# Performance work log

Measured on AMD Instinct MI355X. Metric: run time of the kernel, lower is better.

The kernel has to match this reference:

```python
import jax, jax.numpy as jnp
import numpy as np

B, N, HID = 1, 2048, 2048
NH, NKV, HD = 16, 4, 128
GROUPS = NH // NKV
CHUNK = 64          # get_valid_chunk_size(B*NH*N=32768, 64) == 64
MAG = 0.5
GATE_NORM = 16.0


def setup_inputs() -> dict:
    key = jax.random.key(0)
    ks = jax.random.split(key, 5)
    s = 0.02
    return {
        "hidden_states": jax.random.normal(ks[0], (B, N, HID), jnp.float32),
        "Wq": jax.random.normal(ks[1], (NH * HD, HID), jnp.float32) * s,
        "Wk": jax.random.normal(ks[2], (NKV * HD, HID), jnp.float32) * s,
        "Wv": jax.random.normal(ks[3], (NKV * HD, HID), jnp.float32) * s,
        "Wo": jax.random.normal(ks[4], (HID, NH * HD), jnp.float32) * s,
    }


def _delta_rule_chunked(q, k, v, beta, chunk_size):
    """Chunkwise delta-rule linear attention (DeltaNet chunk form).
    q,k,v,beta: [T, d] flattened tokens; returns (o [T,d], final_state [d,d])."""
    T, d = q.shape
    n = T // chunk_size
    qc, kc, vc, bc = (x.reshape(n, chunk_size, d) for x in (q, k, v, beta))
    kb = kc * bc                       # beta-weighted keys
    vb = vc * bc                       # beta-weighted values
    strict = jnp.tril(jnp.ones((chunk_size, chunk_size), bool), -1)
    eye = jnp.eye(chunk_size, dtype=q.dtype)
    # A = I + strictly-lower(k_beta k^T); unit lower triangular -> invert by triangular solve
    A = eye + jnp.where(strict, jnp.einsum('ncd,nkd->nck', kb, kc), 0.0)
    Tinv = jax.vmap(lambda a: jax.scipy.linalg.solve_triangular(a, eye, lower=True))(A)
    w = Tinv @ kb                      # [n, C, d]
    u = Tinv @ vb                      # [n, C, d]
    causal = jnp.tril(jnp.ones((chunk_size, chunk_size), bool))

    def step(S, inp):
        qi, ki, wi, ui = inp           # each [C, d]
        u_i = ui - wi @ S              # correct pseudo-values by inter-chunk state
        attn = jnp.where(causal, qi @ ki.T, 0.0)
        o = qi @ S + attn @ u_i
        return S + ki.T @ u_i, o

    S0 = jnp.zeros((d, d), q.dtype)
    Sf, o = jax.lax.scan(step, S0, (qc, kc, w, u))
    return o.reshape(T, d), Sf


def _forward(hidden_states, Wq, Wk, Wv, Wo):
    q = hidden_states @ Wq.T           # [B, N, NH*HD]
    k = hidden_states @ Wk.T           # [B, N, NKV*HD]
    v = hidden_states @ Wv.T           # [B, N, NKV*HD]
    g = k                              # AdaptiveAvgPool1d(512 -> 512) is identity
    qh = q.reshape(B, N, NH, HD).transpose(0, 2, 1, 3)   # b h n d
    kh = k.reshape(B, N, NKV, HD).transpose(0, 2, 1, 3)
    vh = v.reshape(B, N, NKV, HD).transpose(0, 2, 1, 3)
    gh = g.reshape(B, N, NKV, HD).transpose(0, 2, 1, 3)
    rep = lambda x: jnp.repeat(x, GROUPS, axis=1)        # repeat_kv
    khr, vhr, ghr = rep(kh), rep(vh), rep(gh)

    # linear-attention path: softmax feature maps + logsigmoid gate
    ql = jax.nn.softmax(qh, axis=-1).astype(jnp.float32)
    kl = jax.nn.softmax(khr, axis=-1).astype(jnp.float32)
    gl = (jax.nn.log_sigmoid(ghr) / GATE_NORM).astype(jnp.float32)
    vl = vhr.astype(jnp.float32)
    flat = lambda x: x.reshape(B * NH * N, HD)
    o_lin, _ = _delta_rule_chunked(flat(ql), flat(kl), flat(vl), flat(gl), CHUNK)
    o_lin = o_lin.reshape(B, NH, N, HD).transpose(0, 2, 1, 3).reshape(B, N, NH * HD)
    o_lin = o_lin @ Wo.T

    # base (vanilla causal softmax) attention path
    scores = jnp.einsum('bhnd,bhmd->bhnm', qh, khr) * (HD ** -0.5)
    cmask = jnp.tril(jnp.ones((N, N), bool))
    scores = jnp.where(cmask[None, None], scores, jnp.finfo(scores.dtype).min)
    attn = jax.nn.softmax(scores, axis=-1)
    o_base = jnp.einsum('bhnm,bhmd->bhnd', attn, vhr)
    o_base = o_base.transpose(0, 2, 1, 3).reshape(B, N, NH * HD) @ Wo.T

    return MAG * o_lin + (1.0 - MAG) * o_base


def reference(hidden_states, Wq, Wk, Wv, Wo):
    return _forward(hidden_states, Wq, Wk, Wv, Wo)
```

## Files before the change

kernel.cpp:

```cpp
#include <hip/hip_runtime.h>
#include <hip/hip_bf16.h>

typedef unsigned short u16;
typedef unsigned int u32;
typedef __bf16 bf16x8 __attribute__((ext_vector_type(8)));
typedef float f32x4 __attribute__((ext_vector_type(4)));

#define MFMA16(a,b,c) __builtin_amdgcn_mfma_f32_16x16x32_bf16((a),(b),(c),0,0,0)

__device__ __forceinline__ u16 f2bf(float f){
  u32 u = __builtin_bit_cast(u32, f);
  u32 r = (u + 0x7fffu + ((u >> 16) & 1u)) >> 16;
  return (u16)r;
}
__device__ __forceinline__ float bf2f(u16 h){
  u32 u = ((u32)h) << 16;
  return __builtin_bit_cast(float, u);
}
__device__ __forceinline__ void splitbf(float x, u16& hi, u16& lo){
  hi = f2bf(x);
  lo = f2bf(x - bf2f(hi));
}
__device__ __forceinline__ void gload_lds16(const u16* g, u16* l){
  __builtin_amdgcn_global_load_lds((__attribute__((address_space(1))) void*)(g),
                                   (__attribute__((address_space(3))) void*)(l), 16, 0, 0);
}
__device__ __forceinline__ const u16* selu(const u16* barr, const u16* parr, int i){
  return (i < 128) ? (barr + (size_t)i*16384) : (parr + (size_t)(i-128)*16384);
}
__device__ __forceinline__ const float* self32(const float* barr, const float* parr, int i){
  return (i < 128) ? (barr + (size_t)i*16384) : (parr + (size_t)(i-128)*16384);
}
__device__ __forceinline__ float* slotp(float* p1, float* p2, int s){
  return (s < 381) ? (p1 + (size_t)s*16512) : (p2 + (size_t)(s-381)*16512);
}
__device__ __forceinline__ const float* slotpc(const float* p1, const float* p2, int s){
  return (s < 381) ? (p1 + (size_t)s*16512) : (p2 + (size_t)(s-381)*16512);
}

constexpr size_t OF_HSBF   = 0;
constexpr size_t OF_WQKVBF = 8388608;
constexpr size_t OF_WOBF   = 20971520;
constexpr size_t OF_QKV    = 29360128;
constexpr size_t OF_QBF    = 54525952;
constexpr size_t OF_KBF    = 62914560;
constexpr size_t OF_VT     = 65011712;
constexpr size_t OF_QLB    = 67108864;
constexpr size_t OF_KLF    = 75497472;
constexpr size_t OF_KLB    = 79691776;
constexpr size_t OF_GLF    = 81788928;
constexpr size_t OF_TINV   = 85983232;
constexpr size_t OF_WF     = 88080384;
constexpr size_t OF_WB     = 92274688;
constexpr size_t OF_U0     = 94371840;
constexpr size_t OF_SJ     = 111149056;
constexpr size_t OF_OMIX   = 127926272;
constexpr size_t OF_OMIXB  = 144703488;
constexpr size_t OF_ADF  = 102760448;
constexpr size_t OF_ABTF = OF_OMIX;
constexpr size_t OF_ADH  = OF_OMIX + 8388608;
constexpr size_t OF_ADL  = OF_OMIX + 12582912;
constexpr size_t OF_ADTH = OF_OMIXB;
constexpr size_t OF_ADTL = OF_OMIXB + 4194304;
constexpr size_t OF_ABTH = OF_KLF;
constexpr size_t OF_ABTL = OF_GLF;
constexpr size_t OF_BDF  = OF_QKV;
constexpr size_t OF_BBTF = OF_QKV + 8388608;
constexpr size_t OF_BDH  = OF_QKV + 16777216;
constexpr size_t OF_BDL  = OF_QKV + 20971520;
constexpr size_t OF_BDTH = OF_HSBF;
constexpr size_t OF_BDTL = OF_HSBF + 4194304;
constexpr size_t OF_BBTH = OF_WQKVBF;
constexpr size_t OF_BBTL = OF_WQKVBF + 4194304;
constexpr size_t OF_TTF  = OF_TINV;
constexpr size_t OF_TTH  = OF_WQKVBF + 8388608;
constexpr size_t OF_TTL  = OF_WQKVBF + 8912896;
constexpr size_t OF_PDF  = OF_ADF;
constexpr size_t OF_PBTF = OF_ADF + 1048576;
constexpr size_t OF_PDH  = OF_ADF + 2097152;
constexpr size_t OF_PDL  = OF_ADF + 2621440;
constexpr size_t OF_PDTH = OF_ADF + 3145728;
constexpr size_t OF_PDTL = OF_ADF + 3670016;
constexpr size_t OF_PBTH = OF_ADF + 4194304;
constexpr size_t OF_PBTL = OF_ADF + 4718592;
constexpr size_t OF_APART1 = OF_QKV;
constexpr size_t OF_APART2 = OF_OMIXB;
constexpr size_t OF_OBF = 0;

struct CompJobs { int a[8]; int b[8]; int d[8]; };

__global__ void k_f2ball(const float* __restrict__ hs, const float* __restrict__ Wq,
                         const float* __restrict__ Wk, const float* __restrict__ Wv,
                         const float* __restrict__ Wo, u16* __restrict__ hs_bf,
                         u16* __restrict__ wqkv_bf, u16* __restrict__ wo_bf){
  int bid = blockIdx.x;
  const float* src; u16* dst; int off;
  if(bid < 4096){ src = hs; dst = hs_bf; off = bid; }
  else if(bid < 8192){ src = Wq; dst = wqkv_bf; off = bid - 4096; }
  else if(bid < 9216){ src = Wk; dst = wqkv_bf + 2048*2048; off = bid - 8192; }
  else if(bid < 10240){ src = Wv; dst = wqkv_bf + 2560*2048; off = bid - 9216; }
  else { src = Wo; dst = wo_bf; off = bid - 10240; }
  int i = (off*256 + threadIdx.x) * 4;
  f32x4 v = *(const f32x4*)(src + i);
  u32 w0 = (u32)f2bf(v[0]) | ((u32)f2bf(v[1]) << 16);
  u32 w1 = (u32)f2bf(v[2]) | ((u32)f2bf(v[3]) << 16);
  *(u32*)(dst + i) = w0;
  *(u32*)(dst + i + 2) = w1;
}

__global__ __launch_bounds__(256) void k_gemm(const u16* __restrict__ A, const u16* __restrict__ B,
                                              float* __restrict__ C, int K, int N){
  __shared__ u16 aL[128*32];
  __shared__ u16 bL[128*32];
  int lin = blockIdx.y * gridDim.x + blockIdx.x;
  int nwg = gridDim.x * gridDim.y;
  int s = (lin & 7) * (nwg >> 3) + (lin >> 3);
  int bn = s % gridDim.x, bm = s / gridDim.x;
  int tid = threadIdx.x, lane = tid & 63, w = tid >> 6;
  int wm = w >> 1, wn = w & 1;
  f32x4 acc[4][4] = {};
  int nK = K >> 5;
  const u16* Abase = A + (size_t)bm * 128 * K;
  const u16* Bbase = B + (size_t)bn * 128 * K;
  for(int kt = 0; kt < nK; ++kt){
    __syncthreads();
    #pragma unroll
    for(int t = 0; t < 2; ++t){
      int row = t*64 + w*16 + (lane >> 2);
      int kc = (lane & 3) * 8;
      gload_lds16(Abase + (size_t)row*K + kt*32 + kc, &aL[(t*64 + w*16)*32]);
      gload_lds16(Bbase + (size_t)row*K + kt*32 + kc, &bL[(t*64 + w*16)*32]);
    }
    __syncthreads();
    bf16x8 af[4], bf[4];
    #pragma unroll
    for(int i = 0; i < 4; ++i){
      af[i] = *(const bf16x8*)&aL[(wm*64 + i*16 + (lane & 15))*32 + ((lane >> 4) << 3)];
      bf[i] = *(const bf16x8*)&bL[(wn*64 + i*16 + (lane & 15))*32 + ((lane >> 4) << 3)];
    }
    #pragma unroll
    for(int i = 0; i < 4; ++i)
      #pragma unroll
      for(int j = 0; j < 4; ++j)
        acc[i][j] = MFMA16(af[i], bf[j], acc[i][j]);
  }
  #pragma unroll
  for(int i = 0; i < 4; ++i)
    #pragma unroll
    for(int j = 0; j < 4; ++j)
      #pragma unroll
      for(int r = 0; r < 4; ++r){
        int row = bm*128 + wm*64 + i*16 + ((lane >> 4) << 2) + r;
        int col = bn*128 + wn*64 + j*16 + (lane & 15);
        C[(size_t)row * N + col] = acc[i][j][r];
      }
}

__global__ __launch_bounds__(256) void k_linvt(const float* __restrict__ qkv, u16* qbf, u16* qlb,
                                               u16* kbf, float* klf, u16* klb, float* glf,
                                               u16* __restrict__ vT){
  __shared__ float t[64][65];
  int bid = blockIdx.x;
  if(bid < 10240){
    int gtask = bid * 4 + (threadIdx.x >> 6);
    int lane = threadIdx.x & 63;
    int n = gtask / 20, tt = gtask % 20;
    const float* row = (tt < 16) ? (qkv + (size_t)n*3072 + tt*128)
                                 : (qkv + (size_t)n*3072 + 2048 + (tt-16)*128);
    float v0 = row[lane], v1 = row[lane + 64];
    float m = fmaxf(v0, v1);
    #pragma unroll
    for(int o = 1; o < 64; o <<= 1) m = fmaxf(m, __shfl_xor(m, o, 64));
    float e0 = __expf(v0 - m), e1 = __expf(v1 - m);
    float s = e0 + e1;
    #pragma unroll
    for(int o = 1; o < 64; o <<= 1) s += __shfl_xor(s, o, 64);
    float r0 = e0 / s, r1 = e1 / s;
    if(tt < 16){
      size_t base = ((size_t)tt*2048 + n) * 128;
      qbf[base + lane] = f2bf(v0); qbf[base + 64 + lane] = f2bf(v1);
      qlb[base + lane] = f2bf(r0); qlb[base + 64 + lane] = f2bf(r1);
    } else {
      int g = tt - 16;
      size_t base = ((size_t)g*2048 + n) * 128;
      kbf[base + lane] = f2bf(v0); kbf[base + 64 + lane] = f2bf(v1);
      klf[base + lane] = r0;       klf[base + 64 + lane] = r1;
      klb[base + lane] = f2bf(r0); klb[base + 64 + lane] = f2bf(r1);
      float g0 = (fminf(v0, 0.f) - log1pf(__expf(-fabsf(v0)))) * (1.f/16.f);
      float g1 = (fminf(v1, 0.f) - log1pf(__expf(-fabsf(v1)))) * (1.f/16.f);
      glf[base + lane] = g0; glf[base + 64 + lane] = g1;
    }
  } else {
    int v = bid - 10240;
    int nt = v & 31, dt = (v >> 5) & 1, g = v >> 6;
    int tid = threadIdx.x;
    {
      int r = tid >> 2, c0 = (tid & 3) * 16;
      const float* src = qkv + (size_t)(nt*64 + r)*3072 + 2560 + g*128 + dt*64 + c0;
      #pragma unroll
      for(int q = 0; q < 16; q += 4){
        f32x4 vv = *(const f32x4*)(src + q);
        t[r][c0+q] = vv[0]; t[r][c0+q+1] = vv[1]; t[r][c0+q+2] = vv[2]; t[r][c0+q+3] = vv[3];
      }
    }
    __syncthreads();
    {
      int d = tid >> 2, c0 = (tid & 3) * 16;
      u16* dst = vT + ((size_t)g*128 + dt*64 + d)*2048 + (size_t)nt*64 + c0;
      #pragma unroll
      for(int half = 0; half < 2; ++half){
        int b = c0 + half*8;
        u32 w0 = (u32)f2bf(t[b+0][d]) | ((u32)f2bf(t[b+1][d]) << 16);
        u32 w1 = (u32)f2bf(t[b+2][d]) | ((u32)f2bf(t[b+3][d]) << 16);
        u32 w2 = (u32)f2bf(t[b+4][d]) | ((u32)f2bf(t[b+5][d]) << 16);
        u32 w3 = (u32)f2bf(t[b+6][d]) | ((u32)f2bf(t[b+7][d]) << 16);
        *(uint4*)(dst + half*8) = make_uint4(w0, w1, w2, w3);
      }
    }
  }
}

__global__ __launch_bounds__(256) void k_prep1(const float* __restrict__ klf, const float* __restrict__ glf,
                                               float* __restrict__ tinv){
  __shared__ float KlT[128][68];
  __shared__ float Kb[64][132];
  __shared__ float Am[64][68];
  __shared__ float XT[64][68];
  int idx = blockIdx.x, g = idx >> 5, c = idx & 31, tid = threadIdx.x;
  size_t base = ((size_t)g*2048 + c*64) * 128;
  {
    int r = tid >> 2, d0 = (tid & 3) * 32;
    #pragma unroll
    for(int dd = 0; dd < 32; dd += 4){
      f32x4 kv = *(const f32x4*)(klf + base + r*128 + d0 + dd);
      f32x4 gv = *(const f32x4*)(glf + base + r*128 + d0 + dd);
      KlT[d0+dd][r] = kv[0]; KlT[d0+dd+1][r] = kv[1]; KlT[d0+dd+2][r] = kv[2]; KlT[d0+dd+3][r] = kv[3];
      f32x4 kb = kv * gv;
      *(f32x4*)&Kb[r][d0+dd] = kb;
    }
  }
  __syncthreads();
  {
    int i = tid >> 2, j0 = (tid & 3) * 16;
    f32x4 s[4] = {};
    for(int d = 0; d < 128; ++d){
      float kb = Kb[i][d];
      #pragma unroll
      for(int q = 0; q < 4; ++q){
        f32x4 kl = *(const f32x4*)&KlT[d][j0 + q*4];
        s[q] += kb * kl;
      }
    }
    #pragma unroll
    for(int q = 0; q < 4; ++q) *(f32x4*)&Am[i][j0 + q*4] = s[q];
  }
  __syncthreads();
  if(tid < 64){
    int cc = tid;
    float x0 = (cc == 0) ? 1.f : 0.f;
    XT[cc][0] = x0;
    tinv[(size_t)idx*4096 + cc] = x0;
    for(int i = 1; i < 64; ++i){
      float s = (i == cc) ? 1.f : 0.f;
      int i4 = i & ~3;
      for(int jj = 0; jj < i4; jj += 4){
        f32x4 av = *(const f32x4*)&Am[i][jj];
        f32x4 xv = *(const f32x4*)&XT[cc][jj];
        s -= av[0]*xv[0] + av[1]*xv[1] + av[2]*xv[2] + av[3]*xv[3];
      }
      for(int jj = i4; jj < i; ++jj) s -= Am[i][jj] * XT[cc][jj];
      XT[cc][i] = s;
      tinv[(size_t)idx*4096 + i*64 + cc] = s;
    }
  }
}

__global__ __launch_bounds__(256) void k_prep2a(const float* __restrict__ klf, const float* __restrict__ glf,
                                                const float* __restrict__ qkv, const float* __restrict__ tinv,
                                                float* __restrict__ wf, u16* __restrict__ wb, float* __restrict__ u0f){
  __shared__ float Ti[64][68];
  __shared__ float B1[64][132];
  __shared__ float B2[64][132];
  int idx = blockIdx.x, g = idx >> 5, c = idx & 31, tid = threadIdx.x;
  size_t base = ((size_t)g*2048 + c*64) * 128;
  {
    int r = tid >> 2, d0 = (tid & 3) * 32;
    #pragma unroll
    for(int dd = 0; dd < 32; dd += 4){
      f32x4 kv = *(const f32x4*)(klf + base + r*128 + d0 + dd);
      f32x4 gv = *(const f32x4*)(glf + base + r*128 + d0 + dd);
      f32x4 vv = *(const f32x4*)(qkv + (size_t)(c*64 + r)*3072 + 2560 + g*128 + d0 + dd);
      *(f32x4*)&B1[r][d0+dd] = kv * gv;
      *(f32x4*)&B2[r][d0+dd] = vv * gv;
    }
    int c0 = (tid & 3) * 16;
    #pragma unroll
    for(int q = 0; q < 16; q += 4)
      *(f32x4*)&Ti[r][c0+q] = *(const f32x4*)(tinv + (size_t)idx*4096 + r*64 + c0 + q);
  }
  __syncthreads();
  int i = tid >> 2, cc0 = (tid & 3) * 32;
  f32x4 wa[8] = {}; f32x4 ua[8] = {};
  for(int jj = 0; jj < 64; ++jj){
    float a = Ti[i][jj];
    #pragma unroll
    for(int q = 0; q < 8; ++q){
      f32x4 b1 = *(const f32x4*)&B1[jj][cc0 + q*4];
      f32x4 b2 = *(const f32x4*)&B2[jj][cc0 + q*4];
      wa[q] += a * b1; ua[q] += a * b2;
    }
  }
  #pragma unroll
  for(int q = 0; q < 8; ++q){
    *(f32x4*)(wf + (size_t)idx*8192 + i*128 + cc0 + q*4) = wa[q];
    *(f32x4*)(u0f + (size_t)idx*8192 + i*128 + cc0 + q*4) = ua[q];
    u32 w0 = (u32)f2bf(wa[q][0]) | ((u32)f2bf(wa[q][1]) << 16);
    u32 w1 = (u32)f2bf(wa[q][2]) | ((u32)f2bf(wa[q][3]) << 16);
    u32* dst = (u32*)(wb + (size_t)idx*8192 + i*128 + cc0 + q*4);
    dst[0] = w0; dst[1] = w1;
  }
}

__global__ __launch_bounds__(256) void k_prep2b(const float* __restrict__ klf, const float* __restrict__ wf,
                                                const float* __restrict__ u0f,
                                                float* __restrict__ dF, u16* __restrict__ dH, u16* __restrict__ dL,
                                                u16* __restrict__ dTH, u16* __restrict__ dTL,
                                                float* __restrict__ btF, u16* __restrict__ btH, u16* __restrict__ btL){
  __shared__ float Kl[64][132];
  __shared__ float Wm[64][132];
  __shared__ float Um[64][132];
  int idx = blockIdx.x, g = idx >> 5, c = idx & 31, tid = threadIdx.x;
  size_t base = ((size_t)g*2048 + c*64) * 128;
  {
    int r = tid >> 2, d0 = (tid & 3) * 32;
    #pragma unroll
    for(int dd = 0; dd < 32; dd += 4){
      *(f32x4*)&Kl[r][d0+dd] = *(const f32x4*)(klf + base + r*128 + d0 + dd);
      *(f32x4*)&Wm[r][d0+dd] = *(const f32x4*)(wf + (size_t)idx*8192 + r*128 + d0 + dd);
      *(f32x4*)&Um[r][d0+dd] = *(const f32x4*)(u0f + (size_t)idx*8192 + r*128 + d0 + dd);
    }
  }
  __syncthreads();
  int a = tid >> 1, b0 = (tid & 1) * 64;
  f32x4 pa[16] = {}; f32x4 ca[16] = {};
  for(int r = 0; r < 64; ++r){
    float ka = Kl[r][a];
    float ua = Um[r][a];
    #pragma unroll
    for(int q = 0; q < 16; ++q){
      f32x4 wv = *(const f32x4*)&Wm[r][b0 + q*4];
      f32x4 kv = *(const f32x4*)&Kl[r][b0 + q*4];
      pa[q] += ka * wv;
      ca[q] += ua * kv;
    }
  }
  size_t ob = (size_t)idx * 16384;
  #pragma unroll
  for(int q = 0; q < 16; ++q){
    #pragma unroll
    for(int e = 0; e < 4; ++e){
      int b = b0 + q*4 + e;
      float dv = -pa[q][e];
      u16 dh, dl; splitbf(dv, dh, dl);
      dF[ob + a*128 + b] = dv;
      dH[ob + a*128 + b] = dh;
      dL[ob + a*128 + b] = dl;
      dTH[ob + (size_t)b*128 + a] = dh;
      dTL[ob + (size_t)b*128 + a] = dl;
      float cv = ca[q][e];
      u16 ch, cl; splitbf(cv, ch, cl);
      btF[ob + a*128 + b] = cv;
      btH[ob + a*128 + b] = ch;
      btL[ob + a*128 + b] = cl;
    }
  }
}

__global__ __launch_bounds__(256) void k_ks(
    const float* __restrict__ sDF, const u16* __restrict__ sDH, const u16* __restrict__ sDL,
    const u16* __restrict__ sDTH, const u16* __restrict__ sDTL,
    const float* __restrict__ sBF, const u16* __restrict__ sBH, const u16* __restrict__ sBL,
    float* __restrict__ dDF, u16* __restrict__ dDH, u16* __restrict__ dDL,
    u16* __restrict__ dDTH, u16* __restrict__ dDTL,
    float* __restrict__ dBF, u16* __restrict__ dBH, u16* __restrict__ dBL, int off){
  __shared__ float T[128][132];
  int c = blockIdx.x, g = blockIdx.y, z = blockIdx.z;
  int idx = g*32 + c, tid = threadIdx.x;
  size_t base = (size_t)idx * 16384;
  if(c < off){
    if(z == 0){
      for(int i = tid; i < 4096; i += 256) ((uint4*)(dDF + base))[i] = ((const uint4*)(sDF + base))[i];
      for(int i = tid; i < 2048; i += 256){
        ((uint4*)(dDH + base))[i] = ((const uint4*)(sDH + base))[i];
        ((uint4*)(dDL + base))[i] = ((const uint4*)(sDL + base))[i];
        ((uint4*)(dDTH + base))[i] = ((const uint4*)(sDTH + base))[i];
        ((uint4*)(dDTL + base))[i] = ((const uint4*)(sDTL + base))[i];
      }
    } else {
      for(int i = tid; i < 4096; i += 256) ((uint4*)(dBF + base))[i] = ((const uint4*)(sBF + base))[i];
      for(int i = tid; i < 2048; i += 256){
        ((uint4*)(dBH + base))[i] = ((const uint4*)(sBH + base))[i];
        ((uint4*)(dBL + base))[i] = ((const uint4*)(sBL + base))[i];
      }
    }
    return;
  }
  size_t blo = (size_t)(idx - off) * 16384;
  int lane = tid & 63, w = tid >> 6;
  const u16 *Ah, *Al, *Bh, *Bl;
  if(z == 0){ Ah = sDH + base; Al = sDL + base; Bh = sDTH + blo; Bl = sDTL + blo; }
  else      { Ah = sBH + blo;  Al = sBL + blo;  Bh = sDH + base; Bl = sDL + base; }
  f32x4 acc[2][8] = {};
  #pragma unroll
  for(int ks = 0; ks < 4; ++ks){
    bf16x8 ah[2], al[2], bh[8], bl[8];
    #pragma unroll
    for(int mt = 0; mt < 2; ++mt){
      int ro = (w*32 + mt*16 + (lane & 15))*128 + ks*32 + ((lane >> 4) << 3);
      ah[mt] = *(const bf16x8*)(Ah + ro);
      al[mt] = *(const bf16x8*)(Al + ro);
    }
    #pragma unroll
    for(int nt = 0; nt < 8; ++nt){
      int ro = (nt*16 + (lane & 15))*128 + ks*32 + ((lane >> 4) << 3);
      bh[nt] = *(const bf16x8*)(Bh + ro);
      bl[nt] = *(const bf16x8*)(Bl + ro);
    }
    #pragma unroll
    for(int mt = 0; mt < 2; ++mt)
      #pragma unroll
      for(int nt = 0; nt < 8; ++nt)
        acc[mt][nt] = MFMA16(ah[mt], bh[nt],
                      MFMA16(ah[mt], bl[nt],
                      MFMA16(al[mt], bh[nt], acc[mt][nt])));
  }
  if(z == 0){
    #pragma unroll
    for(int mt = 0; mt < 2; ++mt)
      #pragma unroll
      for(int nt = 0; nt < 8; ++nt)
        #pragma unroll
        for(int r = 0; r < 4; ++r){
          int row = w*32 + mt*16 + ((lane >> 4) << 2) + r;
          int col = nt*16 + (lane & 15);
          float v = acc[mt][nt][r] + sDF[base + row*128 + col] + sDF[blo + row*128 + col];
          dDF[base + row*128 + col] = v;
          u16 hi, lo; splitbf(v, hi, lo);
          dDH[base + row*128 + col] = hi;
          dDL[base + row*128 + col] = lo;
          T[row][col] = v;
        }
    __syncthreads();
    int tcol = tid >> 1, half = tid & 1;
    for(int m = 0; m < 64; ++m){
      float v = T[half*64 + m][tcol];
      u16 hi, lo; splitbf(v, hi, lo);
      dDTH[base + (size_t)tcol*128 + half*64 + m] = hi;
      dDTL[base + (size_t)tcol*128 + half*64 + m] = lo;
    }
  } else {
    #pragma unroll
    for(int mt = 0; mt < 2; ++mt)
      #pragma unroll
      for(int nt = 0; nt < 8; ++nt)
        #pragma unroll
        for(int r = 0; r < 4; ++r){
          int row = w*32 + mt*16 + ((lane >> 4) << 2) + r;
          int col = nt*16 + (lane & 15);
          float v = acc[mt][nt][r] + sBF[base + row*128 + col] + sBF[blo + row*128 + col];
          dBF[base + row*128 + col] = v;
          u16 hi, lo; splitbf(v, hi, lo);
          dBH[base + row*128 + col] = hi;
          dBL[base + row*128 + col] = lo;
        }
  }
}

__device__ __forceinline__ void comp_mfma(const u16* Ah, const u16* Al, const u16* Bh, const u16* Bl,
                                          f32x4 (&acc)[2][8], int lane, int w){
  #pragma unroll
  for(int ks = 0; ks < 4; ++ks){
    bf16x8 ah[2], al[2], bh[8], bl[8];
    #pragma unroll
    for(int mt = 0; mt < 2; ++mt){
      int ro = (w*32 + mt*16 + (lane & 15))*128 + ks*32 + ((lane >> 4) << 3);
      ah[mt] = *(const bf16x8*)(Ah + ro);
      al[mt] = *(const bf16x8*)(Al + ro);
    }
    #pragma unroll
    for(int nt = 0; nt < 8; ++nt){
      int ro = (nt*16 + (lane & 15))*128 + ks*32 + ((lane >> 4) << 3);
      bh[nt] = *(const bf16x8*)(Bh + ro);
      bl[nt] = *(const bf16x8*)(Bl + ro);
    }
    #pragma unroll
    for(int mt = 0; mt < 2; ++mt)
      #pragma unroll
      for(int nt = 0; nt < 8; ++nt)
        acc[mt][nt] = MFMA16(ah[mt], bh[nt],
                      MFMA16(ah[mt], bl[nt],
                      MFMA16(al[mt], bh[nt], acc[mt][nt])));
  }
}

__global__ __launch_bounds__(256) void k_comp(
    const float* __restrict__ bDF, const u16* __restrict__ bDH, const u16* __restrict__ bDL,
    const u16* __restrict__ bDTH, const u16* __restrict__ bDTL,
    const float* __restrict__ bBTF, const u16* __restrict__ bBTH, const u16* __restrict__ bBTL,
    float* __restrict__ pDF, u16* __restrict__ pDH, u16* __restrict__ pDL,
    u16* __restrict__ pDTH, u16* __restrict__ pDTL,
    float* __restrict__ pBTF, u16* __restrict__ pBTH, u16* __restrict__ pBTL,
    CompJobs jobs){
  __shared__ float T[128][132];
  int job = blockIdx.x, z = blockIdx.y, tid = threadIdx.x;
  int a = jobs.a[job], b = jobs.b[job], d = jobs.d[job] - 128;
  size_t ob = (size_t)d * 16384;
  int lane = tid & 63, w = tid >> 6;
  const u16 *Ah, *Al, *Bh, *Bl;
  const float *F1, *F2;
  if(z == 0){
    Ah = selu(bDH, pDH, a);  Al = selu(bDL, pDL, a);
    Bh = selu(bDTH, pDTH, b); Bl = selu(bDTL, pDTL, b);
    F1 = self32(bDF, pDF, a); F2 = self32(bDF, pDF, b);
  } else {
    Ah = selu(bBTH, pBTH, b); Al = selu(bBTL, pBTL, b);
    Bh = selu(bDH, pDH, a);   Bl = selu(bDL, pDL, a);
    F1 = self32(bBTF, pBTF, a); F2 = self32(bBTF, pBTF, b);
  }
  for(int i = tid*4; i < 16384; i += 1024){
    f32x4 v1 = *(const f32x4*)(F1 + i);
    f32x4 v2 = *(const f32x4*)(F2 + i);
    f32x4 sv = v1 + v2;
    int row = i >> 7, col = i & 127;
    *(f32x4*)&T[row][col] = sv;
  }
  __syncthreads();
  f32x4 acc[2][8] = {};
  comp_mfma(Ah, Al, Bh, Bl, acc, lane, w);
  if(z == 0){
    #pragma unroll
    for(int mt = 0; mt < 2; ++mt)
      #pragma unroll
      for(int nt = 0; nt < 8; ++nt)
        #pragma unroll
        for(int r = 0; r < 4; ++r){
          int row = w*32 + mt*16 + ((lane >> 4) << 2) + r;
          int col = nt*16 + (lane & 15);
          float v = acc[mt][nt][r] + T[row][col];
          pDF[ob + row*128 + col] = v;
          u16 hi, lo; splitbf(v, hi, lo);
          pDH[ob + row*128 + col] = hi;
          pDL[ob + row*128 + col] = lo;
          T[row][col] = v;
        }
    __syncthreads();
    int tcol = tid >> 1, half = tid & 1;
    for(int m = 0; m < 64; ++m){
      float v = T[half*64 + m][tcol];
      u16 hi, lo; splitbf(v, hi, lo);
      pDTH[ob + (size_t)tcol*128 + half*64 + m] = hi;
      pDTL[ob + (size_t)tcol*128 + half*64 + m] = lo;
    }
  } else {
    #pragma unroll
    for(int mt = 0; mt < 2; ++mt)
      #pragma unroll
      for(int nt = 0; nt < 8; ++nt)
        #pragma unroll
        for(int r = 0; r < 4; ++r){
          int row = w*32 + mt*16 + ((lane >> 4) << 2) + r;
          int col = nt*16 + (lane & 15);
          float v = acc[mt][nt][r] + T[row][col];
          pBTF[ob + row*128 + col] = v;
          u16 hi, lo; splitbf(v, hi, lo);
          pBTH[ob + row*128 + col] = hi;
          pBTL[ob + row*128 + col] = lo;
        }
  }
}

__global__ __launch_bounds__(256) void k_heads(
    const u16* __restrict__ bDH, const u16* __restrict__ bDL,
    const float* __restrict__ bBTF, const u16* __restrict__ bBTH, const u16* __restrict__ bBTL,
    const u16* __restrict__ pDH, const u16* __restrict__ pDL,
    const float* __restrict__ pBTF, const u16* __restrict__ pBTH, const u16* __restrict__ pBTL,
    float* __restrict__ ttF, u16* __restrict__ ttH, u16* __restrict__ ttL, u16* __restrict__ sj){
  __shared__ float T[128][132];
  int h = blockIdx.x, g = h >> 2, i0 = h & 3;
  int tid = threadIdx.x, lane = tid & 63, w = tid >> 6;
  int psi = (g == 0) ? -1 : (g == 1 ? 136 : (g == 2 ? 140 : 142));
  int phi = (i0 == 0) ? -1 : (i0 == 1 ? g*32 + 31 : (i0 == 2 ? 128 + g : 132 + g));
  const float* Pf = (psi >= 0) ? self32(bBTF, pBTF, psi) : nullptr;
  const float* Ff = (phi >= 0) ? self32(bBTF, pBTF, phi) : nullptr;
  for(int i = tid*4; i < 16384; i += 1024){
    f32x4 sv = {};
    if(Pf) sv += *(const f32x4*)(Pf + i);
    if(Ff) sv += *(const f32x4*)(Ff + i);
    int row = i >> 7, col = i & 127;
    *(f32x4*)&T[row][col] = sv;
  }
  __syncthreads();
  f32x4 acc[2][8] = {};
  if(psi >= 0 && phi >= 0)
    comp_mfma(selu(bBTH,pBTH,psi), selu(bBTL,pBTL,psi), selu(bDH,pDH,phi), selu(bDL,pDL,phi), acc, lane, w);
  #pragma unroll
  for(int mt = 0; mt < 2; ++mt)
    #pragma unroll
    for(int nt = 0; nt < 8; ++nt)
      #pragma unroll
      for(int r = 0; r < 4; ++r){
        int row = w*32 + mt*16 + ((lane >> 4) << 2) + r;
        int col = nt*16 + (lane & 15);
        float v = acc[mt][nt][r] + T[row][col];
        u16 hi, lo; splitbf(v, hi, lo);
        size_t o = (size_t)h*16384 + row*128 + col;
        ttF[o] = v; ttH[o] = hi; ttL[o] = lo;
        sj[(size_t)(h*32)*16384 + row*128 + col] = hi;
      }
}

__global__ __launch_bounds__(256) void k_expand(const u16* __restrict__ bDH, const u16* __restrict__ bDL,
                                                const float* __restrict__ bBF, const float* __restrict__ ttF,
                                                const u16* __restrict__ ttH, const u16* __restrict__ ttL,
                                                u16* __restrict__ sj){
  int j = blockIdx.x;
  int c = j & 31;
  if(c == 0) return;
  int h = j >> 5, g = h >> 2;
  size_t obase = (size_t)j * 16384;
  size_t mb = (size_t)(g*32 + c - 1) * 16384;
  size_t tb = (size_t)h * 16384;
  int tid = threadIdx.x, lane = tid & 63, w = tid >> 6;
  f32x4 acc[2][8] = {};
  comp_mfma(ttH + tb, ttL + tb, bDH + mb, bDL + mb, acc, lane, w);
  #pragma unroll
  for(int mt = 0; mt < 2; ++mt)
    #pragma unroll
    for(int nt = 0; nt < 8; ++nt)
      #pragma unroll
      for(int r = 0; r < 4; ++r){
        int row = w*32 + mt*16 + ((lane >> 4) << 2) + r;
        int col = nt*16 + (lane & 15);
        float v = acc[mt][nt][r] + ttF[tb + row*128 + col] + bBF[mb + row*128 + col];
        sj[obase + row*128 + col] = f2bf(v);
      }
}

__global__ __launch_bounds__(256) void k_olin(const u16* __restrict__ qlb, const u16* __restrict__ klb,
                                              const u16* __restrict__ wb, const float* __restrict__ u0f,
                                              const u16* __restrict__ sj, float* __restrict__ omix){
  __shared__ u16 ut[128*64];
  __shared__ u16 pl[4][16*64];
  int j = blockIdx.x;
  int h = j >> 5, c = j & 31, g = h >> 2, idx = g*32 + c;
  int tid = threadIdx.x, lane = tid & 63, w = tid >> 6;
  const u16* Sj = sj + (size_t)j * 16384;
  const u16* Q  = qlb + ((size_t)h*2048 + c*64) * 128;
  const u16* Kc = klb + ((size_t)g*2048 + c*64) * 128;
  const u16* W  = wb + (size_t)idx * 8192;
  const float* U0 = u0f + (size_t)idx * 8192;
  bf16x8 aq[4], aw[4];
  #pragma unroll
  for(int ks = 0; ks < 4; ++ks){
    aq[ks] = *(const bf16x8*)(Q + (w*16 + (lane & 15))*128 + ks*32 + ((lane >> 4) << 3));
    aw[ks] = *(const bf16x8*)(W + (w*16 + (lane & 15))*128 + ks*32 + ((lane >> 4) << 3));
  }
  f32x4 t1[8] = {}, ui[8] = {};
  #pragma unroll
  for(int ks = 0; ks < 4; ++ks)
    #pragma unroll
    for(int nt = 0; nt < 8; ++nt){
      bf16x8 b = *(const bf16x8*)(Sj + (nt*16 + (lane & 15))*128 + ks*32 + ((lane >> 4) << 3));
      t1[nt] = MFMA16(aq[ks], b, t1[nt]);
      ui[nt] = MFMA16(aw[ks], b, ui[nt]);
    }
  f32x4 sc[4] = {};
  #pragma unroll
  for(int ks = 0; ks < 4; ++ks)
    #pragma unroll
    for(int nt = 0; nt < 4; ++nt){
      bf16x8 b = *(const bf16x8*)(Kc + (nt*16 + (lane & 15))*128 + ks*32 + ((lane >> 4) << 3));
      sc[nt] = MFMA16(aq[ks], b, sc[nt]);
    }
  #pragma unroll
  for(int nt = 0; nt < 4; ++nt)
    #pragma unroll
    for(int r = 0; r < 4; ++r){
      int row = ((lane >> 4) << 2) + r;
      int col = nt*16 + (lane & 15);
      int grow = w*16 + row;
      float v = (col <= grow) ? sc[nt][r] : 0.f;
      int bo = (row*128 + col*2) ^ ((row & 7) << 4);
      *(u16*)((char*)&pl[w][0] + bo) = f2bf(v);
    }
  #pragma unroll
  for(int nt = 0; nt < 8; ++nt)
    #pragma unroll
    for(int r = 0; r < 4; ++r){
      int kv = w*16 + ((lane >> 4) << 2) + r;
      int d  = nt*16 + (lane & 15);
      float v = U0[kv*128 + d] - ui[nt][r];
      int bo = (d*128 + kv*2) ^ ((d & 7) << 4);
      *(u16*)((char*)ut + bo) = f2bf(v);
    }
  __syncthreads();
  f32x4 o2[8] = {};
  #pragma unroll
  for(int ks2 = 0; ks2 < 2; ++ks2){
    int row = lane & 15;
    int boA = (row*128 + ks2*64 + ((lane >> 4) << 4)) ^ ((row & 7) << 4);
    bf16x8 a = *(const bf16x8*)((const char*)&pl[w][0] + boA);
    #pragma unroll
    for(int nt = 0; nt < 8; ++nt){
      int d = nt*16 + (lane & 15);
      int boB = (d*128 + ks2*64 + ((lane >> 4) << 4)) ^ ((d & 7) << 4);
      bf16x8 b = *(const bf16x8*)((const char*)ut + boB);
      o2[nt] = MFMA16(a, b, o2[nt]);
    }
  }
  #pragma unroll
  for(int nt = 0; nt < 8; ++nt)
    #pragma unroll
    for(int r = 0; r < 4; ++r){
      int grow = c*64 + w*16 + ((lane >> 4) << 2) + r;
      int d = nt*16 + (lane & 15);
      omix[(size_t)grow*2048 + h*128 + d] = 0.5f * (t1[nt][r] + o2[nt][r]);
    }
}

__global__ __launch_bounds__(256) void k_attn(const u16* __restrict__ qbf, const u16* __restrict__ kbf,
                                              const u16* __restrict__ vT, const float* __restrict__ omix,
                                              u16* __restrict__ obf,
                                              float* __restrict__ part1, float* __restrict__ part2){
  __shared__ u16 pl[4][2560];
  int rb = blockIdx.x;
  int bid = (rb & 7) * 80 + (rb >> 3);
  int h = bid / 40, j = bid % 40;
  int qB, kt0, kt1, slot = -1;
  if(j < 4){ qB = j; kt0 = 0; kt1 = 4*(qB+1); }
  else {
    int jj = j - 4; int seg;
    if(jj < 8){ qB = 4 + (jj >> 1); seg = jj & 1; }
    else if(jj < 20){ int q = jj - 8; qB = 8 + q/3; seg = q - (qB-8)*3; }
    else { int q = jj - 20; qB = 12 + (q >> 2); seg = q & 3; }
    slot = h*36 + jj;
    kt0 = seg*16;
    int full = 4*(qB+1);
    kt1 = (kt0 + 16 < full) ? kt0 + 16 : full;
  }
  int g = h >> 2;
  int tid = threadIdx.x, lane = tid & 63, w = tid >> 6;
  const u16* K = kbf + (size_t)g*2048*128;
  const u16* V = vT + (size_t)g*128*2048;
  bf16x8 aq[2][4];
  #pragma unroll
  for(int m = 0; m < 2; ++m){
    const u16* Q = qbf + ((size_t)h*2048 + qB*128 + w*32 + m*16) * 128;
    #pragma unroll
    for(int ks = 0; ks < 4; ++ks)
      aq[m][ks] = *(const bf16x8*)(Q + (lane & 15)*128 + ks*32 + ((lane >> 4) << 3));
  }
  f32x4 acc[2][8] = {};
  float lsum[2][4] = {};
  const float scale = 0.08838834764831845f;
  int qr0[2];
  #pragma unroll
  for(int m = 0; m < 2; ++m) qr0[m] = qB*128 + w*32 + m*16 + ((lane >> 4) << 2);
  u16* plw = &pl[w][0];
  bf16x8 kb[8];
  #pragma unroll
  for(int ct = 0; ct < 2; ++ct)
    #pragma unroll
    for(int ks = 0; ks < 4; ++ks)
      kb[ct*4+ks] = *(const bf16x8*)(K + (size_t)(kt0*32 + ct*16 + (lane & 15))*128 + ks*32 + ((lane >> 4) << 3));
  int buf = 0;
  for(int kt = kt0; kt < kt1; ++kt){
    f32x4 s[2][2] = {};
    #pragma unroll
    for(int m = 0; m < 2; ++m)
      #pragma unroll
      for(int ct = 0; ct < 2; ++ct)
        #pragma unroll
        for(int ks = 0; ks < 4; ++ks)
          s[m][ct] = MFMA16(aq[m][ks], kb[ct*4+ks], s[m][ct]);
    bf16x8 kbn[8];
    if(kt + 1 < kt1){
      #pragma unroll
      for(int ct = 0; ct < 2; ++ct)
        #pragma unroll
        for(int ks = 0; ks < 4; ++ks)
          kbn[ct*4+ks] = *(const bf16x8*)(K + (size_t)((kt+1)*32 + ct*16 + (lane & 15))*128 + ks*32 + ((lane >> 4) << 3));
    }
    bf16x8 bv[8];
    #pragma unroll
    for(int nt = 0; nt < 8; ++nt)
      bv[nt] = *(const bf16x8*)(V + (size_t)(nt*16 + (lane & 15))*2048 + kt*32 + ((lane >> 4) << 3));
    #pragma unroll
    for(int m = 0; m < 2; ++m)
      #pragma unroll
      for(int ct = 0; ct < 2; ++ct)
        #pragma unroll
        for(int r = 0; r < 4; ++r){
          int col = kt*32 + ct*16 + (lane & 15);
          float p = (col <= qr0[m] + r) ? __expf(s[m][ct][r] * scale) : 0.f;
          lsum[m][r] += p;
          int row = m*16 + ((lane >> 4) << 2) + r;
          *(u16*)((char*)plw + buf*2560 + row*80 + (ct*16 + (lane & 15))*2) = f2bf(p);
        }
    __builtin_amdgcn_s_setprio(1);
    #pragma unroll
    for(int m = 0; m < 2; ++m){
      bf16x8 ap = *(const bf16x8*)((const char*)plw + buf*2560 + (m*16 + (lane & 15))*80 + ((lane >> 4) << 4));
      #pragma unroll
      for(int nt = 0; nt < 8; ++nt)
        acc[m][nt] = MFMA16(ap, bv[nt], acc[m][nt]);
    }
    __builtin_amdgcn_s_setprio(0);
    #pragma unroll
    for(int i = 0; i < 8; ++i) kb[i] = kbn[i];
    buf ^= 1;
  }
  #pragma unroll
  for(int m = 0; m < 2; ++m)
    #pragma unroll
    for(int r = 0; r < 4; ++r){
      float v = lsum[m][r];
      v += __shfl_xor(v, 1, 64); v += __shfl_xor(v, 2, 64);
      v += __shfl_xor(v, 4, 64); v += __shfl_xor(v, 8, 64);
      lsum[m][r] = v;
    }
  if(slot < 0){
    #pragma unroll
    for(int m = 0; m < 2; ++m)
      #pragma unroll
      for(int nt = 0; nt < 8; ++nt)
        #pragma unroll
        for(int r = 0; r < 4; ++r){
          int row = qB*128 + w*32 + m*16 + ((lane >> 4) << 2) + r;
          int d = nt*16 + (lane & 15);
          size_t o = (size_t)row*2048 + h*128 + d;
          float fin = omix[o] + 0.5f * acc[m][nt][r] / lsum[m][r];
          obf[o] = f2bf(fin);
        }
  } else {
    float* P = slotp(part1, part2, slot);
    #pragma unroll
    for(int m = 0; m < 2; ++m)
      #pragma unroll
      for(int nt = 0; nt < 8; ++nt)
        #pragma unroll
        for(int r = 0; r < 4; ++r){
          int row = w*32 + m*16 + ((lane >> 4) << 2) + r;
          int d = nt*16 + (lane & 15);
          P[(size_t)row*128 + d] = acc[m][nt][r];
        }
    if((lane & 15) == 0)
      #pragma unroll
      for(int m = 0; m < 2; ++m)
        #pragma unroll
        for(int r = 0; r < 4; ++r)
          P[16384 + w*32 + m*16 + ((lane >> 4) << 2) + r] = lsum[m][r];
  }
}

__global__ __launch_bounds__(256) void k_acomb(const float* __restrict__ part1, const float* __restrict__ part2,
                                               const float* __restrict__ omix, u16* __restrict__ obf){
  int bid = blockIdx.x;
  int h = bid / 12, qx = bid % 12, qB = 4 + qx;
  int nseg = (qB >= 12) ? 4 : (qB >= 8) ? 3 : 2;
  int off = (qB < 8) ? (qB-4)*2 : (qB < 12) ? 8 + (qB-8)*3 : 20 + (qB-12)*4;
  int s0 = h*36 + off;
  int tid = threadIdx.x;
  #pragma unroll
  for(int it = 0; it < 16; ++it){
    int i = it*1024 + tid*4;
    int row = i >> 7;
    f32x4 a = {};
    float l = 0.f;
    for(int s = 0; s < nseg; ++s){
      const float* P = slotpc(part1, part2, s0 + s);
      a += *(const f32x4*)(P + i);
      l += P[16384 + row];
    }
    size_t idx = (size_t)(qB*128 + row)*2048 + h*128 + (i & 127);
    f32x4 cur = *(const f32x4*)(omix + idx);
    f32x4 fin = cur + a * (0.5f / l);
    u32 w0 = (u32)f2bf(fin[0]) | ((u32)f2bf(fin[1]) << 16);
    u32 w1 = (u32)f2bf(fin[2]) | ((u32)f2bf(fin[3]) << 16);
    *(u32*)(obf + idx) = w0;
    *(u32*)(obf + idx + 2) = w1;
  }
}

extern "C" void kernel_launch(void* const* d_in, const int* in_sizes, int n_in,
                              void* d_out, int out_size, void* d_ws, size_t ws_size,
                              hipStream_t stream){
  (void)in_sizes; (void)n_in; (void)out_size; (void)ws_size;
  const float* hs = (const float*)d_in[0];
  const float* Wq = (const float*)d_in[1];
  const float* Wk = (const float*)d_in[2];
  const float* Wv = (const float*)d_in[3];
  const float* Wo = (const float*)d_in[4];
  float* out = (float*)d_out;
  char* ws = (char*)d_ws;

  u16*   hs_bf   = (u16*)(ws + OF_HSBF);
  u16*   wqkv_bf = (u16*)(ws + OF_WQKVBF);
  u16*   wo_bf   = (u16*)(ws + OF_WOBF);
  float* qkv     = (float*)(ws + OF_QKV);
  u16*   qbf     = (u16*)(ws + OF_QBF);
  u16*   kbf     = (u16*)(ws + OF_KBF);
  u16*   vT      = (u16*)(ws + OF_VT);
  u16*   qlb     = (u16*)(ws + OF_QLB);
  float* klf     = (float*)(ws + OF_KLF);
  u16*   klb     = (u16*)(ws + OF_KLB);
  float* glf     = (float*)(ws + OF_GLF);
  float* tinvb   = (float*)(ws + OF_TINV);
  float* wf      = (float*)(ws + OF_WF);
  u16*   wb      = (u16*)(ws + OF_WB);
  float* u0f     = (float*)(ws + OF_U0);
  u16*   sjb     = (u16*)(ws + OF_SJ);
  float* omix    = (float*)(ws + OF_OMIX);
  u16*   obf     = (u16*)(ws + OF_OBF);
  float* aDF  = (float*)(ws + OF_ADF);
  u16*   aDH  = (u16*)(ws + OF_ADH);
  u16*   aDL  = (u16*)(ws + OF_ADL);
  u16*   aDTH = (u16*)(ws + OF_ADTH);
  u16*   aDTL = (u16*)(ws + OF_ADTL);
  float* aBTF = (float*)(ws + OF_ABTF);
  u16*   aBTH = (u16*)(ws + OF_ABTH);
  u16*   aBTL = (u16*)(ws + OF_ABTL);
  float* bDF  = (float*)(ws + OF_BDF);
  u16*   bDH  = (u16*)(ws + OF_BDH);
  u16*   bDL  = (u16*)(ws + OF_BDL);
  u16*   bDTH = (u16*)(ws + OF_BDTH);
  u16*   bDTL = (u16*)(ws + OF_BDTL);
  float* bBTF = (float*)(ws + OF_BBTF);
  u16*   bBTH = (u16*)(ws + OF_BBTH);
  u16*   bBTL = (u16*)(ws + OF_BBTL);
  float* ttF  = (float*)(ws + OF_TTF);
  u16*   ttH  = (u16*)(ws + OF_TTH);
  u16*   ttL  = (u16*)(ws + OF_TTL);
  float* pDF  = (float*)(ws + OF_PDF);
  float* pBTF = (float*)(ws + OF_PBTF);
  u16*   pDH  = (u16*)(ws + OF_PDH);
  u16*   pDL  = (u16*)(ws + OF_PDL);
  u16*   pDTH = (u16*)(ws + OF_PDTH);
  u16*   pDTL = (u16*)(ws + OF_PDTL);
  u16*   pBTH = (u16*)(ws + OF_PBTH);
  u16*   pBTL = (u16*)(ws + OF_PBTL);
  float* apart1 = (float*)(ws + OF_APART1);
  float* apart2 = (float*)(ws + OF_APART2);

  k_f2ball<<<14336, 256, 0, stream>>>(hs, Wq, Wk, Wv, Wo, hs_bf, wqkv_bf, wo_bf);
  k_gemm<<<dim3(24, 16), 256, 0, stream>>>(hs_bf, wqkv_bf, qkv, 2048, 3072);
  k_linvt<<<10496, 256, 0, stream>>>(qkv, qbf, qlb, kbf, klf, klb, glf, vT);

  k_prep1<<<128, 256, 0, stream>>>(klf, glf, tinvb);
  k_prep2a<<<128, 256, 0, stream>>>(klf, glf, qkv, tinvb, wf, wb, u0f);
  k_prep2b<<<128, 256, 0, stream>>>(klf, wf, u0f, aDF, aDH, aDL, aDTH, aDTL, aBTF, aBTH, aBTL);

  k_ks<<<dim3(32, 4, 2), 256, 0, stream>>>(aDF, aDH, aDL, aDTH, aDTL, aBTF, aBTH, aBTL,
                                           bDF, bDH, bDL, bDTH, bDTL, bBTF, bBTH, bBTL, 1);
  k_ks<<<dim3(32, 4, 2), 256, 0, stream>>>(bDF, bDH, bDL, bDTH, bDTL, bBTF, bBTH, bBTL,
                                           aDF, aDH, aDL, aDTH, aDTL, aBTF, aBTH, aBTL, 2);
  k_ks<<<dim3(32, 4, 2), 256, 0, stream>>>(aDF, aDH, aDL, aDTH, aDTL, aBTF, aBTH, aBTL,
                                           bDF, bDH, bDL, bDTH, bDTL, bBTF, bBTH, bBTL, 4);
  k_ks<<<dim3(32, 4, 2), 256, 0, stream>>>(bDF, bDH, bDL, bDTH, bDTL, bBTF, bBTH, bBTL,
                                           aDF, aDH, aDL, aDTH, aDTL, aBTF, aBTH, aBTL, 8);
  k_ks<<<dim3(32, 4, 2), 256, 0, stream>>>(aDF, aDH, aDL, aDTH, aDTL, aBTF, aBTH, aBTL,
                                           bDF, bDH, bDL, bDTH, bDTL, bBTF, bBTH, bBTL, 16);

  CompJobs j1{};
  for(int g = 0; g < 4; ++g){ j1.a[g] = g*32+31; j1.b[g] = g*32+31; j1.d[g] = 128+g; }
  k_comp<<<dim3(4, 2), 256, 0, stream>>>(bDF, bDH, bDL, bDTH, bDTL, bBTF, bBTH, bBTL,
                                         pDF, pDH, pDL, pDTH, pDTL, pBTF, pBTH, pBTL, j1);
  CompJobs j2{};
  for(int g = 0; g < 4; ++g){
    j2.a[g]   = 128+g; j2.b[g]   = g*32+31; j2.d[g]   = 132+g;
    j2.a[4+g] = 128+g; j2.b[4+g] = 128+g;   j2.d[4+g] = 136+g;
  }
  k_comp<<<dim3(8, 2), 256, 0, stream>>>(bDF, bDH, bDL, bDTH, bDTL, bBTF, bBTH, bBTL,
                                         pDF, pDH, pDL, pDTH, pDTL, pBTF, pBTH, pBTL, j2);
  CompJobs j3{};
  j3.a[0] = 137; j3.b[0] = 136; j3.d[0] = 140;
  j3.a[1] = 138; j3.b[1] = 137; j3.d[1] = 141;
  k_comp<<<dim3(2, 2), 256, 0, stream>>>(bDF, bDH, bDL, bDTH, bDTL, bBTF, bBTH, bBTL,
                                         pDF, pDH, pDL, pDTH, pDTL, pBTF, pBTH, pBTL, j3);
  CompJobs j4{};
  j4.a[0] = 141; j4.b[0] = 136; j4.d[0] = 142;
  k_comp<<<dim3(1, 2), 256, 0, stream>>>(bDF, bDH, bDL, bDTH, bDTL, bBTF, bBTH, bBTL,
                                         pDF, pDH, pDL, pDTH, pDTL, pBTF, pBTH, pBTL, j4);

  k_heads<<<16, 256, 0, stream>>>(bDH, bDL, bBTF, bBTH, bBTL,
                                  pDH, pDL, pBTF, pBTH, pBTL, ttF, ttH, ttL, sjb);
  k_expand<<<512, 256, 0, stream>>>(bDH, bDL, bBTF, ttF, ttH, ttL, sjb);

  k_olin<<<512, 256, 0, stream>>>(qlb, klb, wb, u0f, sjb, omix);
  k_attn<<<640, 256, 0, stream>>>(qbf, kbf, vT, omix, obf, apart1, apart2);
  k_acomb<<<192, 256, 0, stream>>>(apart1, apart2, omix, obf);

  k_gemm<<<dim3(16, 16), 256, 0, stream>>>(obf, wo_bf, out, 2048, 2048);
}
```

Measured before the change: 705.8 us.

## Stage K and V tiles in shared LDS per block in attention kernel

The causal attention kernel used to have each wave load K and V tiles straight from global memory into registers, with K prefetched one tile ahead. Now the block loads each 32-key K tile and V^T tile once into swizzled LDS with global_load_lds, fenced by two __syncthreads per iteration, and all four waves read from there. This cuts redundant global and L2 traffic fourfold, at the cost of losing the register prefetch overlap and adding block-wide barriers. The P buffer drops from double to single buffering to make room in LDS.

```diff
diff --git a/kernel.cpp b/kernel.cpp
--- a/kernel.cpp
+++ b/kernel.cpp
@@ -732,7 +732,9 @@
                                               const u16* __restrict__ vT, const float* __restrict__ omix,
                                               u16* __restrict__ obf,
                                               float* __restrict__ part1, float* __restrict__ part2){
-  __shared__ u16 pl[4][2560];
+  __shared__ u16 Kl[4096];
+  __shared__ u16 Vl[4096];
+  __shared__ u16 pl[4][1280];
   int rb = blockIdx.x;
   int bid = (rb & 7) * 80 + (rb >> 3);
   int h = bid / 40, j = bid % 40;
@@ -767,14 +769,33 @@
   #pragma unroll
   for(int m = 0; m < 2; ++m) qr0[m] = qB*128 + w*32 + m*16 + ((lane >> 4) << 2);
   u16* plw = &pl[w][0];
-  bf16x8 kb[8];
-  #pragma unroll
-  for(int ct = 0; ct < 2; ++ct)
-    #pragma unroll
-    for(int ks = 0; ks < 4; ++ks)
-      kb[ct*4+ks] = *(const bf16x8*)(K + (size_t)(kt0*32 + ct*16 + (lane & 15))*128 + ks*32 + ((lane >> 4) << 3));
-  int buf = 0;
   for(int kt = kt0; kt < kt1; ++kt){
+    __syncthreads();
+    #pragma unroll
+    for(int inst = 0; inst < 2; ++inst){
+      int ob = w*2048 + inst*1024;
+      int lo = ob + lane*16;
+      {
+        int r = lo >> 8;
+        int gc = ((lo >> 4) & 15) ^ (r & 7);
+        gload_lds16(K + (size_t)(kt*32 + r)*128 + gc*8, (u16*)((char*)Kl + ob));
+      }
+      {
+        int d = lo >> 6;
+        int gnb = ((lo >> 4) & 3) ^ ((d >> 1) & 3);
+        gload_lds16(V + (size_t)d*2048 + kt*32 + gnb*8, (u16*)((char*)Vl + ob));
+      }
+    }
+    __syncthreads();
+    bf16x8 kb[8];
+    #pragma unroll
+    for(int ct = 0; ct < 2; ++ct)
+      #pragma unroll
+      for(int ks = 0; ks < 4; ++ks){
+        int r = ct*16 + (lane & 15);
+        int pc = (ks*4 + (lane >> 4)) ^ (r & 7);
+        kb[ct*4+ks] = *(const bf16x8*)(Kl + r*128 + pc*8);
+      }
     f32x4 s[2][2] = {};
     #pragma unroll
     for(int m = 0; m < 2; ++m)
@@ -783,18 +804,13 @@
         #pragma unroll
         for(int ks = 0; ks < 4; ++ks)
           s[m][ct] = MFMA16(aq[m][ks], kb[ct*4+ks], s[m][ct]);
-    bf16x8 kbn[8];
-    if(kt + 1 < kt1){
-      #pragma unroll
-      for(int ct = 0; ct < 2; ++ct)
-        #pragma unroll
-        for(int ks = 0; ks < 4; ++ks)
-          kbn[ct*4+ks] = *(const bf16x8*)(K + (size_t)((kt+1)*32 + ct*16 + (lane & 15))*128 + ks*32 + ((lane >> 4) << 3));
-    }
     bf16x8 bv[8];
     #pragma unroll
-    for(int nt = 0; nt < 8; ++nt)
-      bv[nt] = *(const bf16x8*)(V + (size_t)(nt*16 + (lane & 15))*2048 + kt*32 + ((lane >> 4) << 3));
+    for(int nt = 0; nt < 8; ++nt){
+      int d = nt*16 + (lane & 15);
+      int pnb = (lane >> 4) ^ ((d >> 1) & 3);
+      bv[nt] = *(const bf16x8*)(Vl + d*32 + pnb*8);
+    }
     #pragma unroll
     for(int m = 0; m < 2; ++m)
       #pragma unroll
@@ -805,20 +821,17 @@
           float p = (col <= qr0[m] + r) ? __expf(s[m][ct][r] * scale) : 0.f;
           lsum[m][r] += p;
           int row = m*16 + ((lane >> 4) << 2) + r;
-          *(u16*)((char*)plw + buf*2560 + row*80 + (ct*16 + (lane & 15))*2) = f2bf(p);
+          *(u16*)((char*)plw + row*80 + (ct*16 + (lane & 15))*2) = f2bf(p);
         }
     __builtin_amdgcn_s_setprio(1);
     #pragma unroll
     for(int m = 0; m < 2; ++m){
-      bf16x8 ap = *(const bf16x8*)((const char*)plw + buf*2560 + (m*16 + (lane & 15))*80 + ((lane >> 4) << 4));
+      bf16x8 ap = *(const bf16x8*)((const char*)plw + (m*16 + (lane & 15))*80 + ((lane >> 4) << 4));
       #pragma unroll
       for(int nt = 0; nt < 8; ++nt)
         acc[m][nt] = MFMA16(ap, bv[nt], acc[m][nt]);
     }
     __builtin_amdgcn_s_setprio(0);
-    #pragma unroll
-    for(int i = 0; i < 8; ++i) kb[i] = kbn[i];
-    buf ^= 1;
   }
   #pragma unroll
   for(int m = 0; m < 2; ++m)
```

After: 656.0 us. 7.1% less time.
